# Kernel tuning notes

Measured on AMD Instinct MI355X. Metric: run time of the kernel, lower is better.

Reference implementation:

```python
import jax, jax.numpy as jnp
import numpy as np

D_MODEL = 2048
NUM_HEADS = 16
D_K = D_MODEL // NUM_HEADS  # 128
D_LATENT = 512
ROPE_DIM = 64
ROPE_BASE = 10000.0


def setup_inputs() -> dict:
    key = jax.random.key(0)
    ks = jax.random.split(key, 16)
    s = 0.02
    return {
        "query_input": jax.random.normal(ks[0], (8, 512, D_MODEL), jnp.float32),
        "kv_input": jax.random.normal(ks[1], (8, 512, D_MODEL), jnp.float32),
        "wq_w": jax.random.normal(ks[2], (D_MODEL, D_MODEL), jnp.float32) * s,
        "wq_b": jnp.zeros((D_MODEL,), jnp.float32),
        "wdkv_w": jax.random.normal(ks[3], (D_LATENT, D_MODEL), jnp.float32) * s,
        "wdkv_b": jnp.zeros((D_LATENT,), jnp.float32),
        "wupk_w": jax.random.normal(ks[4], (D_MODEL, D_LATENT), jnp.float32) * s,
        "wupk_b": jnp.zeros((D_MODEL,), jnp.float32),
        "wupv_w": jax.random.normal(ks[5], (D_MODEL, D_LATENT), jnp.float32) * s,
        "wupv_b": jnp.zeros((D_MODEL,), jnp.float32),
        "wkr_w": jax.random.normal(ks[6], (ROPE_DIM * NUM_HEADS, D_MODEL), jnp.float32) * s,
        "wkr_b": jnp.zeros((ROPE_DIM * NUM_HEADS,), jnp.float32),
        "wo_w": jax.random.normal(ks[7], (D_MODEL, D_MODEL), jnp.float32) * s,
        "wo_b": jnp.zeros((D_MODEL,), jnp.float32),
    }


def _rope(x):
    # x: [B, H, S, R]; apply rotary embedding along last dim
    S, R = x.shape[-2], x.shape[-1]
    inv_freq = 1.0 / (ROPE_BASE ** (jnp.arange(0, R, 2, dtype=jnp.float32) / R))
    t = jnp.arange(S, dtype=jnp.float32)
    freqs = jnp.einsum("i,j->ij", t, inv_freq)          # [S, R/2]
    emb = jnp.concatenate([freqs, freqs], axis=-1)        # [S, R]
    cos, sin = jnp.cos(emb), jnp.sin(emb)
    x1, x2 = x[..., : R // 2], x[..., R // 2 :]
    rot = jnp.concatenate([-x2, x1], axis=-1)
    return x * cos + rot * sin


def reference(query_input, kv_input, wq_w, wq_b, wdkv_w, wdkv_b,
              wupk_w, wupk_b, wupv_w, wupv_b, wkr_w, wkr_b, wo_w, wo_b):
    B, Sq, _ = query_input.shape
    Skv = kv_input.shape[1]
    H, dk, R = NUM_HEADS, D_K, ROPE_DIM

    q = (query_input @ wq_w.T + wq_b).reshape(B, Sq, H, dk).transpose(0, 2, 1, 3)
    c_kv = kv_input @ wdkv_w.T + wdkv_b                   # [B, Skv, L]
    k = (c_kv @ wupk_w.T + wupk_b).reshape(B, Skv, H, dk).transpose(0, 2, 1, 3)
    v = (c_kv @ wupv_w.T + wupv_b).reshape(B, Skv, H, dk).transpose(0, 2, 1, 3)

    k_rope = (kv_input @ wkr_w.T + wkr_b).reshape(B, Skv, H, R).transpose(0, 2, 1, 3)
    k_rope = _rope(k_rope)
    k = jnp.concatenate([k_rope, k[..., R:]], axis=-1)    # overwrite first R dims

    scores = jnp.einsum("bhqd,bhkd->bhqk", q, k) / np.sqrt(dk).astype(jnp.float32)
    attn = jax.nn.softmax(scores, axis=-1)
    context = jnp.einsum("bhqk,bhkd->bhqd", attn, v)
    context = context.transpose(0, 2, 1, 3).reshape(B, Sq, H * dk)
    out = context @ wo_w.T + wo_b
    return out, attn
```

## Files before the change

### kernel.cpp

```cpp
#include <hip/hip_runtime.h>
#include <math.h>

typedef unsigned short u16;
typedef unsigned int   u32;
typedef __attribute__((ext_vector_type(4))) float f32x4;
typedef __attribute__((ext_vector_type(4))) u16   u16x4;
typedef __attribute__((ext_vector_type(8))) __bf16 bf16x8;

#define AS1 __attribute__((address_space(1)))
#define AS3 __attribute__((address_space(3)))

__device__ __forceinline__ u16 f2bf(float f) {
  u32 u = __builtin_bit_cast(u32, f);
  u += 0x7fffu + ((u >> 16) & 1u);
  return (u16)(u >> 16);
}

struct Cast8 {
  const float *i0,*i1,*i2,*i3,*i4,*i5,*i6,*i7;
  u16 *o0,*o1,*o2,*o3,*o4,*o5,*o6,*o7;
};
__global__ void cast_all(Cast8 c) {
  const int i = blockIdx.x * 256 + threadIdx.x;
  if (i >= 7602176) return;
  const float* src = c.i0; u16* dst = c.o0; int off = i;
  if (i >= 2097152 && i < 4194304) { src = c.i1; dst = c.o1; off = i - 2097152; }
  if (i >= 4194304 && i < 5242880) { src = c.i2; dst = c.o2; off = i - 4194304; }
  if (i >= 5242880 && i < 5505024) { src = c.i3; dst = c.o3; off = i - 5242880; }
  if (i >= 5505024 && i < 5767168) { src = c.i4; dst = c.o4; off = i - 5505024; }
  if (i >= 5767168 && i < 6029312) { src = c.i5; dst = c.o5; off = i - 5767168; }
  if (i >= 6029312 && i < 6553600) { src = c.i6; dst = c.o6; off = i - 6029312; }
  if (i >= 6553600)                { src = c.i7; dst = c.o7; off = i - 6553600; }
  f32x4 v = *(const f32x4*)(src + (long)off * 4);
  u16x4 o = { f2bf(v[0]), f2bf(v[1]), f2bf(v[2]), f2bf(v[3]) };
  *(u16x4*)(dst + (long)off * 4) = o;
}

__launch_bounds__(256, 3)
__global__ void gemm_out(const u16* __restrict__ Ag, const u16* __restrict__ Bg,
                         const float* __restrict__ bias, float* __restrict__ C)
{
  __shared__ __align__(16) u16 As[128 * 64];
  __shared__ __align__(16) u16 Bs[128 * 64];
  const int id = blockIdx.x;
  const int tile = (id & 7) * 64 + (id >> 3);
  const int ty = tile >> 4, tx = tile & 15;
  const int m0 = ty << 7, n0 = tx << 7;
  const int tid  = threadIdx.x;
  const int lane = tid & 63;
  const int wid  = tid >> 6;
  const int wm = wid >> 1, wn = wid & 1;
  const int lr = lane & 15, lg = lane >> 4;
  const int rmask = (lr & 7) << 3;

  f32x4 acc[4][4] = {};

  for (int k0 = 0; k0 < 2048; k0 += 64) {
    #pragma unroll
    for (int i = 0; i < 4; ++i) {
      const int eo = tid * 8 + i * 2048;
      const int r = eo >> 6;
      const int cs = (((tid & 7) ^ (r & 7)) << 3);
      __builtin_amdgcn_global_load_lds(
          (const AS1 void*)(Ag + (long)(m0 + r) * 2048 + k0 + cs),
          (AS3 void*)(As + eo), 16, 0, 0);
      __builtin_amdgcn_global_load_lds(
          (const AS1 void*)(Bg + (long)(n0 + r) * 2048 + k0 + cs),
          (AS3 void*)(Bs + eo), 16, 0, 0);
    }
    __syncthreads();
    #pragma unroll
    for (int kk = 0; kk < 64; kk += 32) {
      bf16x8 a4[4], b4[4];
      #pragma unroll
      for (int f = 0; f < 4; ++f)
        a4[f] = *(const bf16x8*)(As + (wm * 64 + f * 16 + lr) * 64 + ((kk + lg * 8) ^ rmask));
      #pragma unroll
      for (int f = 0; f < 4; ++f)
        b4[f] = *(const bf16x8*)(Bs + (wn * 64 + f * 16 + lr) * 64 + ((kk + lg * 8) ^ rmask));
      #pragma unroll
      for (int i = 0; i < 4; ++i)
        #pragma unroll
        for (int j = 0; j < 4; ++j)
          acc[i][j] = __builtin_amdgcn_mfma_f32_16x16x32_bf16(b4[j], a4[i], acc[i][j], 0, 0, 0);
    }
    __syncthreads();
  }

  #pragma unroll
  for (int i = 0; i < 4; ++i) {
    const int R = m0 + wm * 64 + i * 16 + lr;
    #pragma unroll
    for (int j = 0; j < 4; ++j) {
      const int cb = n0 + wn * 64 + j * 16 + lg * 4;
      f32x4 v = acc[i][j];
      f32x4 bv = *(const f32x4*)(bias + cb);
      v[0] += bv[0]; v[1] += bv[1]; v[2] += bv[2]; v[3] += bv[3];
      *(f32x4*)(C + (long)R * 2048 + cb) = v;
    }
  }
}

struct SubG {
  const u16* A; const u16* B; const float* bias; void* C;
  int Nt; int K; int lda; int ldb; int ldc; int EPI; int blk0;
};

__launch_bounds__(256, 3)
__global__ void gemm2(SubG g0, SubG g1, SubG g2, SubG g3, int ng, int nhalf)
{
  __shared__ __align__(16) u16 As[128 * 64];
  __shared__ __align__(16) u16 Bs[128 * 64];
  const int id = blockIdx.x;
  int tile = ((id & 7) * (gridDim.x >> 3)) + (id >> 3);
  if (nhalf > 0) tile = (tile & 1) ? nhalf + (tile >> 1) : (tile >> 1);
  SubG g = g0;
  if (ng > 1 && tile >= g1.blk0) g = g1;
  if (ng > 2 && tile >= g2.blk0) g = g2;
  if (ng > 3 && tile >= g3.blk0) g = g3;
  const int local = tile - g.blk0;
  const int ty = local / g.Nt, tx = local - ty * g.Nt;
  const int m0 = ty << 7, n0 = tx << 7;

  const int tid  = threadIdx.x;
  const int lane = tid & 63;
  const int wid  = tid >> 6;
  const int wm = wid >> 1, wn = wid & 1;
  const int lr = lane & 15, lg = lane >> 4;
  const int lda = g.lda, ldb = g.ldb;
  const bool remapB = (g.EPI == 5);
  const u16* Ag = g.A;
  const u16* Bg = g.B;
  const int rmask = (lr & 7) << 3;

  f32x4 acc[4][4] = {};

  for (int k0 = 0; k0 < g.K; k0 += 64) {
    #pragma unroll
    for (int i = 0; i < 4; ++i) {
      const int eo = tid * 8 + i * 2048;
      const int r = eo >> 6;
      const int cs = (((tid & 7) ^ (r & 7)) << 3);
      __builtin_amdgcn_global_load_lds(
          (const AS1 void*)(Ag + (long)(m0 + r) * lda + (k0 + cs)),
          (AS3 void*)(As + eo), 16, 0, 0);
    }
    #pragma unroll
    for (int i = 0; i < 4; ++i) {
      const int eo = tid * 8 + i * 2048;
      const int r = eo >> 6;
      const int cs = (((tid & 7) ^ (r & 7)) << 3);
      int nr = n0 + r;
      if (remapB) nr = ((nr >> 6) << 7) + 64 + (nr & 63);
      __builtin_amdgcn_global_load_lds(
          (const AS1 void*)(Bg + (long)nr * ldb + (k0 + cs)),
          (AS3 void*)(Bs + eo), 16, 0, 0);
    }
    __syncthreads();
    #pragma unroll
    for (int kk = 0; kk < 64; kk += 32) {
      bf16x8 a4[4], b4[4];
      #pragma unroll
      for (int f = 0; f < 4; ++f)
        a4[f] = *(const bf16x8*)(As + (wm * 64 + f * 16 + lr) * 64 + ((kk + lg * 8) ^ rmask));
      #pragma unroll
      for (int f = 0; f < 4; ++f)
        b4[f] = *(const bf16x8*)(Bs + (wn * 64 + f * 16 + lr) * 64 + ((kk + lg * 8) ^ rmask));
      #pragma unroll
      for (int i = 0; i < 4; ++i)
        #pragma unroll
        for (int j = 0; j < 4; ++j)
          acc[i][j] = __builtin_amdgcn_mfma_f32_16x16x32_bf16(b4[j], a4[i], acc[i][j], 0, 0, 0);
    }
    __syncthreads();
  }

  if (g.EPI == 6) {
    const int h = (n0 + wn * 64) >> 6;
    #pragma unroll
    for (int i = 0; i < 4; ++i) {
      const int R = m0 + wm * 64 + i * 16 + lr;
      const int b = R >> 9, s2 = R & 511;
      const long base = ((long)(b * 16 + h) * 512 + s2) << 7;
      const int msk = (s2 & 7) << 3;
      #pragma unroll
      for (int j = 0; j < 2; ++j) {
        const int cb = n0 + wn * 64 + j * 16 + lg * 4;
        f32x4 b1 = *(const f32x4*)(g.bias + cb);
        f32x4 b2 = *(const f32x4*)(g.bias + cb + 32);
        u16x4 o1, o2;
        #pragma unroll
        for (int rr = 0; rr < 4; ++rr) {
          const int ii = j * 16 + lg * 4 + rr;
          const float invf = __powf(10000.0f, -(float)ii * (1.0f / 32.0f));
          float sn, cs; __sincosf((float)s2 * invf, &sn, &cs);
          const float v1 = acc[i][j][rr] + b1[rr], v2 = acc[i][j + 2][rr] + b2[rr];
          o1[rr] = f2bf(v1 * cs - v2 * sn);
          o2[rr] = f2bf(v2 * cs + v1 * sn);
        }
        const int d1 = j * 16 + lg * 4, d2 = d1 + 32;
        *(u16x4*)((u16*)g.C + base + (d1 ^ msk)) = o1;
        *(u16x4*)((u16*)g.C + base + (d2 ^ msk)) = o2;
      }
    }
  } else {
    #pragma unroll
    for (int i = 0; i < 4; ++i) {
      const int R = m0 + wm * 64 + i * 16 + lr;
      #pragma unroll
      for (int j = 0; j < 4; ++j) {
        const int cb = n0 + wn * 64 + j * 16 + lg * 4;
        f32x4 v = acc[i][j];
        if (g.EPI == 0) {
          if (g.bias) {
            f32x4 bv = *(const f32x4*)(g.bias + cb);
            v[0] += bv[0]; v[1] += bv[1]; v[2] += bv[2]; v[3] += bv[3];
          }
          *(f32x4*)((float*)g.C + (long)R * g.ldc + cb) = v;
        } else if (g.EPI == 1) {
          f32x4 bv = *(const f32x4*)(g.bias + cb);
          u16x4 o = { f2bf(v[0] + bv[0]), f2bf(v[1] + bv[1]),
                      f2bf(v[2] + bv[2]), f2bf(v[3] + bv[3]) };
          *(u16x4*)((u16*)g.C + (long)R * g.ldc + cb) = o;
        } else if (g.EPI == 2) {
          f32x4 bv = *(const f32x4*)(g.bias + cb);
          const int b = R >> 9, s2 = R & 511, h = cb >> 7, d = cb & 127;
          u16x4 o = { f2bf(v[0] + bv[0]), f2bf(v[1] + bv[1]),
                      f2bf(v[2] + bv[2]), f2bf(v[3] + bv[3]) };
          *(u16x4*)((u16*)g.C + (((long)(b * 16 + h) * 512 + s2) << 7) + (d ^ ((s2 & 7) << 3))) = o;
        } else if (g.EPI == 5) {
          const int h = cb >> 6, d = 64 + (cb & 63);
          f32x4 bv = *(const f32x4*)(g.bias + h * 128 + d);
          const int b = R >> 9, s2 = R & 511;
          u16x4 o = { f2bf(v[0] + bv[0]), f2bf(v[1] + bv[1]),
                      f2bf(v[2] + bv[2]), f2bf(v[3] + bv[3]) };
          *(u16x4*)((u16*)g.C + (((long)(b * 16 + h) * 512 + s2) << 7) + (d ^ ((s2 & 7) << 3))) = o;
        } else {
          const int b = R >> 9, s2 = R & 511;
          #pragma unroll
          for (int rr = 0; rr < 4; ++rr) {
            const int cc = cb + rr, h = cc >> 7, d = cc & 127;
            ((u16*)g.C)[(((long)(b * 16 + h) * 128 + d) << 9) + (s2 ^ ((d & 7) << 3))] =
                f2bf(v[rr] + g.bias[cc]);
          }
        }
      }
    }
  }
}

__launch_bounds__(256, 2)
__global__ void fused_attn(const u16* __restrict__ qg, const u16* __restrict__ kg,
                           const u16* __restrict__ vg, float* __restrict__ attn,
                           u16* __restrict__ ctx)
{
  __shared__ __align__(16) u16 Qs[64 * 128];
  __shared__ __align__(16) u16 KVs[128 * 128];
  __shared__ __align__(16) u16 Ps[64 * 128];
  const int tid = threadIdx.x, lane = tid & 63, w = tid >> 6;
  const int lr = lane & 15, lg = lane >> 4;
  const int q0 = blockIdx.x * 64;
  const int bh = blockIdx.y;
  const u16* Qg = qg + ((long)bh * 512 + q0) * 128;
  const u16* Kg = kg + (long)bh * 65536;
  const u16* Vg = vg + (long)bh * 65536;

  #pragma unroll
  for (int i = 0; i < 4; ++i)
    __builtin_amdgcn_global_load_lds((const AS1 void*)(Qg + tid * 8 + i * 2048),
                                     (AS3 void*)(Qs + tid * 8 + i * 2048), 16, 0, 0);

  f32x4 acc[32] = {};
  bf16x8 qa[4];
  const int arow = 16 * w + lr;
  const int amsk = (lr & 7) << 3;

  #pragma unroll
  for (int t = 0; t < 4; ++t) {
    #pragma unroll
    for (int i = 0; i < 8; ++i)
      __builtin_amdgcn_global_load_lds((const AS1 void*)(Kg + t * 16384 + tid * 8 + i * 2048),
                                       (AS3 void*)(KVs + tid * 8 + i * 2048), 16, 0, 0);
    __syncthreads();
    if (t == 0) {
      #pragma unroll
      for (int kc = 0; kc < 4; ++kc)
        qa[kc] = *(const bf16x8*)(Qs + arow * 128 + ((kc * 32 + lg * 8) ^ amsk));
    }
    #pragma unroll
    for (int nf = 0; nf < 8; ++nf) {
      const int n = nf * 16 + lr;
      const int nmsk = (n & 7) << 3;
      #pragma unroll
      for (int kc = 0; kc < 4; ++kc) {
        bf16x8 bb = *(const bf16x8*)(KVs + n * 128 + ((kc * 32 + lg * 8) ^ nmsk));
        acc[t * 8 + nf] = __builtin_amdgcn_mfma_f32_16x16x32_bf16(bb, qa[kc], acc[t * 8 + nf], 0, 0, 0);
      }
    }
    __syncthreads();
  }

  const float scale = 0.08838834764831845f;
  float m_ = -1e30f;
  #pragma unroll
  for (int f = 0; f < 32; ++f)
    #pragma unroll
    for (int r = 0; r < 4; ++r) m_ = fmaxf(m_, acc[f][r]);
  m_ = fmaxf(m_, __shfl_xor(m_, 16));
  m_ = fmaxf(m_, __shfl_xor(m_, 32));
  float s_ = 0.f;
  #pragma unroll
  for (int f = 0; f < 32; ++f)
    #pragma unroll
    for (int r = 0; r < 4; ++r) {
      const float e = __expf((acc[f][r] - m_) * scale);
      acc[f][r] = e; s_ += e;
    }
  s_ += __shfl_xor(s_, 16);
  s_ += __shfl_xor(s_, 32);
  const float inv = 1.0f / s_;
  #pragma unroll
  for (int f = 0; f < 32; ++f)
    #pragma unroll
    for (int r = 0; r < 4; ++r) acc[f][r] *= inv;

  {
    float* arow_p = attn + ((long)bh * 512 + q0 + 16 * w + lr) * 512;
    #pragma unroll
    for (int t = 0; t < 4; ++t)
      #pragma unroll
      for (int gg = 0; gg < 8; ++gg)
        *(f32x4*)(arow_p + t * 128 + gg * 16 + lg * 4) = acc[t * 8 + gg];
  }

  f32x4 ctxa[8] = {};
  #pragma unroll
  for (int t = 0; t < 4; ++t) {
    #pragma unroll
    for (int gg = 0; gg < 8; ++gg) {
      const int col = gg * 16 + lg * 4;
      u16x4 o = { f2bf(acc[t * 8 + gg][0]), f2bf(acc[t * 8 + gg][1]),
                  f2bf(acc[t * 8 + gg][2]), f2bf(acc[t * 8 + gg][3]) };
      *(u16x4*)(Ps + arow * 128 + (col ^ amsk)) = o;
    }
    #pragma unroll
    for (int i = 0; i < 8; ++i) {
      const int eo = tid * 8 + i * 2048;
      __builtin_amdgcn_global_load_lds((const AS1 void*)(Vg + (eo >> 7) * 512 + t * 128 + (eo & 127)),
                                       (AS3 void*)(KVs + eo), 16, 0, 0);
    }
    __syncthreads();
    bf16x8 pa[4];
    #pragma unroll
    for (int kc = 0; kc < 4; ++kc)
      pa[kc] = *(const bf16x8*)(Ps + arow * 128 + ((kc * 32 + lg * 8) ^ amsk));
    #pragma unroll
    for (int nf = 0; nf < 8; ++nf) {
      const int n = nf * 16 + lr;
      const int nmsk = (n & 7) << 3;
      #pragma unroll
      for (int kc = 0; kc < 4; ++kc) {
        bf16x8 vb = *(const bf16x8*)(KVs + n * 128 + ((kc * 32 + lg * 8) ^ nmsk));
        ctxa[nf] = __builtin_amdgcn_mfma_f32_16x16x32_bf16(vb, pa[kc], ctxa[nf], 0, 0, 0);
      }
    }
    __syncthreads();
  }

  const int b = bh >> 4, h = bh & 15;
  u16* crow = ctx + (long)(b * 512 + q0 + 16 * w + lr) * 2048 + h * 128;
  #pragma unroll
  for (int nf = 0; nf < 8; ++nf) {
    u16x4 o = { f2bf(ctxa[nf][0]), f2bf(ctxa[nf][1]),
                f2bf(ctxa[nf][2]), f2bf(ctxa[nf][3]) };
    *(u16x4*)(crow + nf * 16 + lg * 4) = o;
  }
}

extern "C" void kernel_launch(void* const* d_in, const int* in_sizes, int n_in,
                              void* d_out, int out_size, void* d_ws, size_t ws_size,
                              hipStream_t stream)
{
  (void)in_sizes; (void)n_in; (void)out_size; (void)ws_size;
  const float* query  = (const float*)d_in[0];
  const float* kvin   = (const float*)d_in[1];
  const float* wq_w   = (const float*)d_in[2];
  const float* wq_b   = (const float*)d_in[3];
  const float* wdkv_w = (const float*)d_in[4];
  const float* wdkv_b = (const float*)d_in[5];
  const float* wupk_w = (const float*)d_in[6];
  const float* wupk_b = (const float*)d_in[7];
  const float* wupv_w = (const float*)d_in[8];
  const float* wupv_b = (const float*)d_in[9];
  const float* wkr_w  = (const float*)d_in[10];
  const float* wkr_b  = (const float*)d_in[11];
  const float* wo_w   = (const float*)d_in[12];
  const float* wo_b   = (const float*)d_in[13];

  float* out  = (float*)d_out;
  float* attn = out + 8L * 512 * 2048;

  u16* p = (u16*)d_ws;
  u16* query_bf = p; p += 8388608;
  u16* kv_bf    = p; p += 8388608;
  u16* wq_bf    = p; p += 4194304;
  u16* wdkv_bf  = p; p += 1048576;
  u16* wupk_bf  = p; p += 1048576;
  u16* wupv_bf  = p; p += 1048576;
  u16* wkr_bf   = p; p += 2097152;
  u16* wo_bf    = p; p += 4194304;
  u16* q_ws     = p; p += 8388608;
  u16* ckv_bf   = p; p += 2097152;
  u16* k_ws     = p; p += 8388608;
  u16* vT_ws    = p; p += 8388608;
  u16* ctx_ws   = p; p += 8388608;

  Cast8 c8 = { query, kvin, wq_w, wdkv_w, wupk_w, wupv_w, wkr_w, wo_w,
               query_bf, kv_bf, wq_bf, wdkv_bf, wupk_bf, wupv_bf, wkr_bf, wo_bf };
  cast_all<<<dim3(29696), dim3(256), 0, stream>>>(c8);

  SubG gc = { kv_bf, wdkv_bf, wdkv_b, ckv_bf, 4, 2048, 2048, 2048, 512, 1, 0 };
  gemm2<<<dim3(128), dim3(256), 0, stream>>>(gc, gc, gc, gc, 1, 0);

  SubG gq = { query_bf, wq_bf,   wq_b,   q_ws, 16, 2048, 2048, 2048, 0, 2, 0    };
  SubG gr = { kv_bf,    wkr_bf,  wkr_b,  k_ws, 8,  2048, 2048, 2048, 0, 6, 512  };
  SubG gk = { ckv_bf,   wupk_bf, wupk_b, k_ws, 8,  512,  512,  512,  0, 5, 768  };
  SubG gv = { ckv_bf,   wupv_bf, wupv_b, vT_ws,16, 512,  512,  512,  0, 3, 1024 };
  gemm2<<<dim3(1536), dim3(256), 0, stream>>>(gq, gr, gk, gv, 4, 768);

  fused_attn<<<dim3(8, 128, 1), 256, 0, stream>>>(q_ws, k_ws, vT_ws, attn, ctx_ws);

  gemm_out<<<dim3(512), dim3(256), 0, stream>>>(ctx_ws, wo_bf, wo_b, out);
}
```

Before: 279.5 us.

## Double-buffer LDS tiles in GEMM kernels to overlap global loads with MFMA

```diff
diff --git a/kernel.cpp b/kernel.cpp
--- a/kernel.cpp
+++ b/kernel.cpp
@@ -36,12 +36,12 @@
   *(u16x4*)(dst + (long)off * 4) = o;
 }
 
-__launch_bounds__(256, 3)
+__launch_bounds__(256, 2)
 __global__ void gemm_out(const u16* __restrict__ Ag, const u16* __restrict__ Bg,
                          const float* __restrict__ bias, float* __restrict__ C)
 {
-  __shared__ __align__(16) u16 As[128 * 64];
-  __shared__ __align__(16) u16 Bs[128 * 64];
+  __shared__ __align__(16) u16 As[2][128 * 64];
+  __shared__ __align__(16) u16 Bs[2][128 * 64];
   const int id = blockIdx.x;
   const int tile = (id & 7) * 64 + (id >> 3);
   const int ty = tile >> 4, tx = tile & 15;
@@ -53,9 +53,8 @@
   const int lr = lane & 15, lg = lane >> 4;
   const int rmask = (lr & 7) << 3;
 
-  f32x4 acc[4][4] = {};
-
-  for (int k0 = 0; k0 < 2048; k0 += 64) {
+  auto stage = [&](int t, int buf) {
+    const int k0 = t << 6;
     #pragma unroll
     for (int i = 0; i < 4; ++i) {
       const int eo = tid * 8 + i * 2048;
@@ -63,28 +62,43 @@
       const int cs = (((tid & 7) ^ (r & 7)) << 3);
       __builtin_amdgcn_global_load_lds(
           (const AS1 void*)(Ag + (long)(m0 + r) * 2048 + k0 + cs),
-          (AS3 void*)(As + eo), 16, 0, 0);
+          (AS3 void*)(&As[buf][eo]), 16, 0, 0);
       __builtin_amdgcn_global_load_lds(
           (const AS1 void*)(Bg + (long)(n0 + r) * 2048 + k0 + cs),
-          (AS3 void*)(Bs + eo), 16, 0, 0);
-    }
-    __syncthreads();
+          (AS3 void*)(&Bs[buf][eo]), 16, 0, 0);
+    }
+  };
+
+  f32x4 acc[4][4] = {};
+  const int nT = 32;
+  stage(0, 0);
+  for (int t = 0; t < nT; ++t) {
+    const int cur = t & 1;
+    if (t + 1 < nT) {
+      stage(t + 1, cur ^ 1);
+      asm volatile("s_waitcnt vmcnt(8)" ::: "memory");
+    } else {
+      asm volatile("s_waitcnt vmcnt(0)" ::: "memory");
+    }
+    __builtin_amdgcn_s_barrier();
+    __builtin_amdgcn_sched_barrier(0);
     #pragma unroll
     for (int kk = 0; kk < 64; kk += 32) {
       bf16x8 a4[4], b4[4];
       #pragma unroll
       for (int f = 0; f < 4; ++f)
-        a4[f] = *(const bf16x8*)(As + (wm * 64 + f * 16 + lr) * 64 + ((kk + lg * 8) ^ rmask));
+        a4[f] = *(const bf16x8*)(&As[cur][(wm * 64 + f * 16 + lr) * 64 + ((kk + lg * 8) ^ rmask)]);
       #pragma unroll
       for (int f = 0; f < 4; ++f)
-        b4[f] = *(const bf16x8*)(Bs + (wn * 64 + f * 16 + lr) * 64 + ((kk + lg * 8) ^ rmask));
+        b4[f] = *(const bf16x8*)(&Bs[cur][(wn * 64 + f * 16 + lr) * 64 + ((kk + lg * 8) ^ rmask)]);
       #pragma unroll
       for (int i = 0; i < 4; ++i)
         #pragma unroll
         for (int j = 0; j < 4; ++j)
           acc[i][j] = __builtin_amdgcn_mfma_f32_16x16x32_bf16(b4[j], a4[i], acc[i][j], 0, 0, 0);
     }
-    __syncthreads();
+    asm volatile("s_waitcnt lgkmcnt(0)" ::: "memory");
+    __builtin_amdgcn_s_barrier();
   }
 
   #pragma unroll
@@ -106,11 +120,11 @@
   int Nt; int K; int lda; int ldb; int ldc; int EPI; int blk0;
 };
 
-__launch_bounds__(256, 3)
+__launch_bounds__(256, 2)
 __global__ void gemm2(SubG g0, SubG g1, SubG g2, SubG g3, int ng, int nhalf)
 {
-  __shared__ __align__(16) u16 As[128 * 64];
-  __shared__ __align__(16) u16 Bs[128 * 64];
+  __shared__ __align__(16) u16 As[2][128 * 64];
+  __shared__ __align__(16) u16 Bs[2][128 * 64];
   const int id = blockIdx.x;
   int tile = ((id & 7) * (gridDim.x >> 3)) + (id >> 3);
   if (nhalf > 0) tile = (tile & 1) ? nhalf + (tile >> 1) : (tile >> 1);
@@ -133,9 +147,8 @@
   const u16* Bg = g.B;
   const int rmask = (lr & 7) << 3;
 
-  f32x4 acc[4][4] = {};
-
-  for (int k0 = 0; k0 < g.K; k0 += 64) {
+  auto stage = [&](int t, int buf) {
+    const int k0 = t << 6;
     #pragma unroll
     for (int i = 0; i < 4; ++i) {
       const int eo = tid * 8 + i * 2048;
@@ -143,7 +156,7 @@
       const int cs = (((tid & 7) ^ (r & 7)) << 3);
       __builtin_amdgcn_global_load_lds(
           (const AS1 void*)(Ag + (long)(m0 + r) * lda + (k0 + cs)),
-          (AS3 void*)(As + eo), 16, 0, 0);
+          (AS3 void*)(&As[buf][eo]), 16, 0, 0);
     }
     #pragma unroll
     for (int i = 0; i < 4; ++i) {
@@ -154,25 +167,40 @@
       if (remapB) nr = ((nr >> 6) << 7) + 64 + (nr & 63);
       __builtin_amdgcn_global_load_lds(
           (const AS1 void*)(Bg + (long)nr * ldb + (k0 + cs)),
-          (AS3 void*)(Bs + eo), 16, 0, 0);
-    }
-    __syncthreads();
+          (AS3 void*)(&Bs[buf][eo]), 16, 0, 0);
+    }
+  };
+
+  f32x4 acc[4][4] = {};
+  const int nT = g.K >> 6;
+  stage(0, 0);
+  for (int t = 0; t < nT; ++t) {
+    const int cur = t & 1;
+    if (t + 1 < nT) {
+      stage(t + 1, cur ^ 1);
+      asm volatile("s_waitcnt vmcnt(8)" ::: "memory");
+    } else {
+      asm volatile("s_waitcnt vmcnt(0)" ::: "memory");
+    }
+    __builtin_amdgcn_s_barrier();
+    __builtin_amdgcn_sched_barrier(0);
     #pragma unroll
     for (int kk = 0; kk < 64; kk += 32) {
       bf16x8 a4[4], b4[4];
       #pragma unroll
       for (int f = 0; f < 4; ++f)
-        a4[f] = *(const bf16x8*)(As + (wm * 64 + f * 16 + lr) * 64 + ((kk + lg * 8) ^ rmask));
+        a4[f] = *(const bf16x8*)(&As[cur][(wm * 64 + f * 16 + lr) * 64 + ((kk + lg * 8) ^ rmask)]);
       #pragma unroll
       for (int f = 0; f < 4; ++f)
-        b4[f] = *(const bf16x8*)(Bs + (wn * 64 + f * 16 + lr) * 64 + ((kk + lg * 8) ^ rmask));
+        b4[f] = *(const bf16x8*)(&Bs[cur][(wn * 64 + f * 16 + lr) * 64 + ((kk + lg * 8) ^ rmask)]);
       #pragma unroll
       for (int i = 0; i < 4; ++i)
         #pragma unroll
         for (int j = 0; j < 4; ++j)
           acc[i][j] = __builtin_amdgcn_mfma_f32_16x16x32_bf16(b4[j], a4[i], acc[i][j], 0, 0, 0);
     }
-    __syncthreads();
+    asm volatile("s_waitcnt lgkmcnt(0)" ::: "memory");
+    __builtin_amdgcn_s_barrier();
   }
 
   if (g.EPI == 6) {
```

Measured after the change: 298.9 us. 7.0% more time.

## Double-buffer K tiles in fused attention and prefetch first V tile

Applied to the files above, without the earlier changes.

```diff
diff --git a/kernel.cpp b/kernel.cpp
--- a/kernel.cpp
+++ b/kernel.cpp
@@ -254,9 +254,8 @@
                            const u16* __restrict__ vg, float* __restrict__ attn,
                            u16* __restrict__ ctx)
 {
-  __shared__ __align__(16) u16 Qs[64 * 128];
-  __shared__ __align__(16) u16 KVs[128 * 128];
-  __shared__ __align__(16) u16 Ps[64 * 128];
+  __shared__ __align__(16) u16 bufA[128 * 128];
+  __shared__ __align__(16) u16 bufB[128 * 128];
   const int tid = threadIdx.x, lane = tid & 63, w = tid >> 6;
   const int lr = lane & 15, lg = lane >> 4;
   const int q0 = blockIdx.x * 64;
@@ -265,39 +264,66 @@
   const u16* Kg = kg + (long)bh * 65536;
   const u16* Vg = vg + (long)bh * 65536;
 
+  auto stageK = [&](int t, u16* buf) {
+    #pragma unroll
+    for (int i = 0; i < 8; ++i)
+      __builtin_amdgcn_global_load_lds((const AS1 void*)(Kg + t * 16384 + tid * 8 + i * 2048),
+                                       (AS3 void*)(buf + tid * 8 + i * 2048), 16, 0, 0);
+  };
+  auto stageV = [&](int t) {
+    #pragma unroll
+    for (int i = 0; i < 8; ++i) {
+      const int eo = tid * 8 + i * 2048;
+      __builtin_amdgcn_global_load_lds((const AS1 void*)(Vg + (eo >> 7) * 512 + t * 128 + (eo & 127)),
+                                       (AS3 void*)(bufA + eo), 16, 0, 0);
+    }
+  };
+
   #pragma unroll
   for (int i = 0; i < 4; ++i)
     __builtin_amdgcn_global_load_lds((const AS1 void*)(Qg + tid * 8 + i * 2048),
-                                     (AS3 void*)(Qs + tid * 8 + i * 2048), 16, 0, 0);
-
-  f32x4 acc[32] = {};
+                                     (AS3 void*)(bufB + tid * 8 + i * 2048), 16, 0, 0);
+  stageK(0, bufA);
+  __syncthreads();
+
   bf16x8 qa[4];
   const int arow = 16 * w + lr;
   const int amsk = (lr & 7) << 3;
-
+  #pragma unroll
+  for (int kc = 0; kc < 4; ++kc)
+    qa[kc] = *(const bf16x8*)(bufB + arow * 128 + ((kc * 32 + lg * 8) ^ amsk));
+  asm volatile("s_waitcnt lgkmcnt(0)" ::: "memory");
+  __builtin_amdgcn_s_barrier();
+  stageK(1, bufB);
+
+  f32x4 acc[32] = {};
   #pragma unroll
   for (int t = 0; t < 4; ++t) {
-    #pragma unroll
-    for (int i = 0; i < 8; ++i)
-      __builtin_amdgcn_global_load_lds((const AS1 void*)(Kg + t * 16384 + tid * 8 + i * 2048),
-                                       (AS3 void*)(KVs + tid * 8 + i * 2048), 16, 0, 0);
-    __syncthreads();
-    if (t == 0) {
-      #pragma unroll
-      for (int kc = 0; kc < 4; ++kc)
-        qa[kc] = *(const bf16x8*)(Qs + arow * 128 + ((kc * 32 + lg * 8) ^ amsk));
-    }
+    const u16* KV = (t & 1) ? bufB : bufA;
+    __builtin_amdgcn_s_setprio(1);
     #pragma unroll
     for (int nf = 0; nf < 8; ++nf) {
       const int n = nf * 16 + lr;
       const int nmsk = (n & 7) << 3;
       #pragma unroll
       for (int kc = 0; kc < 4; ++kc) {
-        bf16x8 bb = *(const bf16x8*)(KVs + n * 128 + ((kc * 32 + lg * 8) ^ nmsk));
+        bf16x8 bb = *(const bf16x8*)(KV + n * 128 + ((kc * 32 + lg * 8) ^ nmsk));
         acc[t * 8 + nf] = __builtin_amdgcn_mfma_f32_16x16x32_bf16(bb, qa[kc], acc[t * 8 + nf], 0, 0, 0);
       }
     }
-    __syncthreads();
+    __builtin_amdgcn_s_setprio(0);
+    asm volatile("s_waitcnt lgkmcnt(0)" ::: "memory");
+    __builtin_amdgcn_s_barrier();
+    if (t < 3) {
+      if (t + 2 < 4) {
+        stageK(t + 2, (t & 1) ? bufB : bufA);
+        asm volatile("s_waitcnt vmcnt(8)" ::: "memory");
+      } else {
+        asm volatile("s_waitcnt vmcnt(0)" ::: "memory");
+      }
+      __builtin_amdgcn_s_barrier();
+      if (t == 2) stageV(0);
+    }
   }
 
   const float scale = 0.08838834764831845f;
@@ -341,29 +367,26 @@
       const int col = gg * 16 + lg * 4;
       u16x4 o = { f2bf(acc[t * 8 + gg][0]), f2bf(acc[t * 8 + gg][1]),
                   f2bf(acc[t * 8 + gg][2]), f2bf(acc[t * 8 + gg][3]) };
-      *(u16x4*)(Ps + arow * 128 + (col ^ amsk)) = o;
-    }
-    #pragma unroll
-    for (int i = 0; i < 8; ++i) {
-      const int eo = tid * 8 + i * 2048;
-      __builtin_amdgcn_global_load_lds((const AS1 void*)(Vg + (eo >> 7) * 512 + t * 128 + (eo & 127)),
-                                       (AS3 void*)(KVs + eo), 16, 0, 0);
-    }
+      *(u16x4*)(bufB + arow * 128 + (col ^ amsk)) = o;
+    }
+    if (t > 0) stageV(t);
     __syncthreads();
     bf16x8 pa[4];
     #pragma unroll
     for (int kc = 0; kc < 4; ++kc)
-      pa[kc] = *(const bf16x8*)(Ps + arow * 128 + ((kc * 32 + lg * 8) ^ amsk));
+      pa[kc] = *(const bf16x8*)(bufB + arow * 128 + ((kc * 32 + lg * 8) ^ amsk));
+    __builtin_amdgcn_s_setprio(1);
     #pragma unroll
     for (int nf = 0; nf < 8; ++nf) {
       const int n = nf * 16 + lr;
       const int nmsk = (n & 7) << 3;
       #pragma unroll
       for (int kc = 0; kc < 4; ++kc) {
-        bf16x8 vb = *(const bf16x8*)(KVs + n * 128 + ((kc * 32 + lg * 8) ^ nmsk));
+        bf16x8 vb = *(const bf16x8*)(bufA + n * 128 + ((kc * 32 + lg * 8) ^ nmsk));
         ctxa[nf] = __builtin_amdgcn_mfma_f32_16x16x32_bf16(vb, pa[kc], ctxa[nf], 0, 0, 0);
       }
     }
+    __builtin_amdgcn_s_setprio(0);
     __syncthreads();
   }
 
```

New measurement: 279.4 us. About the same (-0.0%).
